# Optimization experiments

Measured on AMD Instinct MI355X. Metric: run time of the kernel, lower is better.

## Reference

```python
import jax, jax.numpy as jnp
import numpy as np

BS, NC, BH, BW, C = 1, 6, 100, 100, 256
HG, WG = 100, 40
HF, WF = 48, 80
HEADS, PTS, HD = 8, 8, 32
MAXOV = 2
NQ = HG * WG


def _nearest_sample(img, grid):
    # img: [B,H,W,Ch], grid: [B,Hg,Wg,2] in [-1,1]; nearest, align_corners=True, zeros padding
    B, H, W, _ = img.shape
    ix = jnp.round((grid[..., 0] + 1.0) * 0.5 * (W - 1))
    iy = jnp.round((grid[..., 1] + 1.0) * 0.5 * (H - 1))
    valid = (ix >= 0) & (ix <= W - 1) & (iy >= 0) & (iy <= H - 1)
    xc = jnp.clip(ix, 0, W - 1).astype(jnp.int32)
    yc = jnp.clip(iy, 0, H - 1).astype(jnp.int32)
    b = jnp.arange(B)[:, None, None]
    return img[b, yc, xc] * valid[..., None]


def _bilinear_sample(img, x, y):
    # img: [B,H,W,Ch]; x,y: [B,N] unnormalized (align_corners=False); zeros padding
    B, H, W, _ = img.shape
    x0 = jnp.floor(x)
    y0 = jnp.floor(y)
    wx1 = x - x0
    wy1 = y - y0
    b = jnp.arange(B)[:, None]

    def corner(xi, yi):
        valid = (xi >= 0) & (xi <= W - 1) & (yi >= 0) & (yi <= H - 1)
        xc = jnp.clip(xi, 0, W - 1).astype(jnp.int32)
        yc = jnp.clip(yi, 0, H - 1).astype(jnp.int32)
        return img[b, yc, xc] * valid[..., None]

    return (corner(x0, y0) * ((1 - wx1) * (1 - wy1))[..., None]
            + corner(x0 + 1, y0) * (wx1 * (1 - wy1))[..., None]
            + corner(x0, y0 + 1) * ((1 - wx1) * wy1)[..., None]
            + corner(x0 + 1, y0 + 1) * (wx1 * wy1)[..., None])


def _forward(query, value, queries_rebatch_grid, restore_bev_grid,
             reference_points_rebatch, bev_pillar_counts, query_pos,
             Wv, bv, Woff, boff, Watt, batt, Wout, bout, spatial_shapes):
    inp_residual = query
    q = query + query_pos                                       # [BS, BH*BW, C]
    # --- rebatch BEV queries per camera via nearest grid_sample ---
    qmap = jnp.broadcast_to(q.reshape(BS, 1, BH, BW, C),
                            (BS, NC, BH, BW, C)).reshape(BS * NC, BH, BW, C)
    q_reb = _nearest_sample(qmap, queries_rebatch_grid).reshape(BS * NC, NQ, C)
    ref = reference_points_rebatch.reshape(BS * NC, NQ, 2)      # flatten(-2): [BNC,NQ,2,1]->[BNC,NQ,2]
    # --- value projection ---
    v = value.transpose(2, 0, 1, 3).reshape(BS * NC, HF * WF, C)
    v = (v @ Wv + bv).reshape(BS * NC, HF, WF, HEADS, HD)
    # --- multi-scale deformable attention (single level) ---
    off = (q_reb @ Woff + boff).reshape(BS * NC, NQ, HEADS, PTS, 2)
    attw = jax.nn.softmax((q_reb @ Watt + batt).reshape(BS * NC, NQ, HEADS, PTS), axis=-1)
    normalizer = jnp.flip(spatial_shapes[0], 0).astype(jnp.float32)  # [WF, HF]
    loc = ref[:, :, None, None, :] + off / normalizer           # [BNC,NQ,HEADS,PTS,2] in [0,1]
    x = (loc[..., 0] * WF - 0.5).transpose(0, 2, 1, 3).reshape(BS * NC * HEADS, NQ * PTS)
    y = (loc[..., 1] * HF - 0.5).transpose(0, 2, 1, 3).reshape(BS * NC * HEADS, NQ * PTS)
    vh = v.transpose(0, 3, 1, 2, 4).reshape(BS * NC * HEADS, HF, WF, HD)
    samp = _bilinear_sample(vh, x, y).reshape(BS * NC, HEADS, NQ, PTS, HD)
    out = jnp.einsum('bhnpd,bnhp->bnhd', samp, attw).reshape(BS * NC, NQ, C)
    queries_out = out.transpose(0, 2, 1)                        # [BNC, C, NQ] (channels-first as module expects)
    # --- restore to BEV feature ---
    qo = queries_out.reshape(BS, NC, C, NQ).transpose(0, 2, 1, 3).reshape(BS, C, NC * HG, WG)
    bevq = _nearest_sample(qo.transpose(0, 2, 3, 1), restore_bev_grid)  # [BS, MAXOV*BH, BW, C]
    bevq = bevq.transpose(0, 3, 1, 2)                           # [BS, C, MAXOV*BH, BW]
    # reshape(BS, C*MAXOV, BH, BW) + all-ones grouped 1x1 conv == sum of the two overlap copies
    slots = bevq[:, :, :BH, :] + bevq[:, :, BH:, :]             # [BS, C, BH, BW]
    slots = slots.reshape(BS, C, BH * BW).transpose(0, 2, 1)    # [BS, BH*BW, C]
    slots = slots * bev_pillar_counts
    slots = slots @ Wout + bout
    return slots + inp_residual  # dropout identity in eval


def setup_inputs():
    key = jax.random.key(0)
    ks = jax.random.split(key, 14)
    s = 1.0 / np.sqrt(C)
    return {
        "query": jax.random.normal(ks[0], (BS, BH * BW, C), jnp.float32),
        "value": jax.random.normal(ks[1], (BS, HF * WF, NC, C), jnp.float32),
        "queries_rebatch_grid": jax.random.uniform(ks[2], (BS * NC, HG, WG, 2), jnp.float32, -1.0, 1.0),
        "restore_bev_grid": jax.random.uniform(ks[3], (BS, MAXOV * BH, BW, 2), jnp.float32, -1.0, 1.0),
        "reference_points_rebatch": jax.random.uniform(ks[4], (BS * NC, NQ, 2, 1), jnp.float32),
        "bev_pillar_counts": jax.random.uniform(ks[5], (BS, BH * BW, 1), jnp.float32),
        "query_pos": jax.random.normal(ks[6], (BS, BH * BW, C), jnp.float32),
        "Wv": jax.random.uniform(ks[7], (C, C), jnp.float32, -s, s),
        "bv": jnp.zeros((C,), jnp.float32),
        "Woff": jax.random.normal(ks[8], (C, HEADS * PTS * 2), jnp.float32) * 0.01,
        "boff": jax.random.uniform(ks[9], (HEADS * PTS * 2,), jnp.float32, -2.0, 2.0),
        "Watt": jax.random.normal(ks[10], (C, HEADS * PTS), jnp.float32) * 0.01,
        "batt": jnp.zeros((HEADS * PTS,), jnp.float32),
        "Wout": jax.random.uniform(ks[11], (C, C), jnp.float32, -s, s),
        "bout": jnp.zeros((C,), jnp.float32),
        "spatial_shapes": jnp.array([[HF, WF]], dtype=jnp.int32),
    }


def reference(query, value, queries_rebatch_grid, restore_bev_grid,
              reference_points_rebatch, bev_pillar_counts, query_pos,
              Wv, bv, Woff, boff, Watt, batt, Wout, bout, spatial_shapes):
    return _forward(query, value, queries_rebatch_grid, restore_bev_grid,
                    reference_points_rebatch, bev_pillar_counts, query_pos,
                    Wv, bv, Woff, boff, Watt, batt, Wout, bout, spatial_shapes)
```

## Files before the change

kernel.cpp:

```cpp
#include <hip/hip_runtime.h>
#include <hip/hip_bf16.h>
#include <math.h>

#define NCAMS 6
#define BH_ 100
#define BW_ 100
#define CDIM 256
#define NQ_ 4000
#define HF_ 48
#define WF_ 80
#define HEADS_ 8
#define PTS_ 8
#define HD_ 32
#define HWV (HF_*WF_)
#define M1_ (NCAMS*HWV)
#define M2_ (NCAMS*NQ_)
#define NOUT_ 10000

#define SA 264
#define SOFF 132
#define SATT 68

typedef __bf16 bf16_t;
typedef __bf16 bf16x8 __attribute__((ext_vector_type(8)));
typedef __bf16 bf16x4 __attribute__((ext_vector_type(4)));
typedef float  f32x4  __attribute__((ext_vector_type(4)));

static __device__ __forceinline__ f32x4 mfma16(bf16x8 a, bf16x8 b, f32x4 c) {
    return __builtin_amdgcn_mfma_f32_16x16x32_bf16(a, b, c, 0, 0, 0);
}

__global__ __launch_bounds__(256) void k0_prep(const float* __restrict__ Wv,
                                               const float* __restrict__ Woff,
                                               const float* __restrict__ Watt,
                                               const float* __restrict__ Wout,
                                               bf16_t* __restrict__ WvT,
                                               bf16_t* __restrict__ WcombT,
                                               bf16_t* __restrict__ WoutT) {
    int b = blockIdx.x, k = threadIdx.x;
    if (b < 256) {
        WvT[b * 256 + k] = (bf16_t)Wv[k * 256 + b];
    } else if (b < 448) {
        int n = b - 256;
        float v = (n < 128) ? Woff[k * 128 + n] : Watt[k * 64 + (n - 128)];
        WcombT[n * 256 + k] = (bf16_t)v;
    } else {
        int n = b - 448;
        WoutT[n * 256 + k] = (bf16_t)Wout[k * 256 + n];
    }
}

__global__ __launch_bounds__(256) void k1_vproj(const float* __restrict__ value,
                                                const bf16_t* __restrict__ WvT,
                                                const float* __restrict__ bv,
                                                bf16_t* __restrict__ vh) {
    __shared__ __align__(16) bf16_t At[32 * SA];
    const int m0 = blockIdx.x * 32;
    const int cam = m0 / HWV;
    const int hw0 = m0 - cam * HWV;
    for (int idx = threadIdx.x; idx < 32 * 64; idx += 256) {
        int r = idx >> 6, c4 = idx & 63;
        float4 v = ((const float4*)value)[((hw0 + r) * NCAMS + cam) * 64 + c4];
        bf16x4 pk; pk[0] = (bf16_t)v.x; pk[1] = (bf16_t)v.y; pk[2] = (bf16_t)v.z; pk[3] = (bf16_t)v.w;
        *(bf16x4*)(At + r * SA + c4 * 4) = pk;
    }
    __syncthreads();
    const int lane = threadIdx.x & 63, w = threadIdx.x >> 6;
    const int lr = lane & 15, lk = lane >> 4;
    f32x4 acc[2][4] = {};
    const bf16_t* a0 = At + lr * SA + lk * 8;
    const bf16_t* b0 = WvT + (w * 64 + lr) * 256 + lk * 8;
#pragma unroll
    for (int ks = 0; ks < 8; ++ks) {
        bf16x8 af[2], bf_[4];
#pragma unroll
        for (int mm = 0; mm < 2; ++mm) af[mm] = *(const bf16x8*)(a0 + mm * 16 * SA + ks * 32);
#pragma unroll
        for (int n = 0; n < 4; ++n) bf_[n] = *(const bf16x8*)(b0 + n * 16 * 256 + ks * 32);
#pragma unroll
        for (int mm = 0; mm < 2; ++mm)
#pragma unroll
            for (int n = 0; n < 4; ++n)
                acc[mm][n] = mfma16(af[mm], bf_[n], acc[mm][n]);
    }
    __syncthreads();
#pragma unroll
    for (int n = 0; n < 4; ++n) {
        int col = w * 64 + n * 16 + lr;
        float bias = bv[col];
#pragma unroll
        for (int mm = 0; mm < 2; ++mm)
#pragma unroll
            for (int j = 0; j < 4; ++j)
                At[(mm * 16 + lk * 4 + j) * SA + col] = (bf16_t)(acc[mm][n][j] + bias);
    }
    __syncthreads();
    for (int idx = threadIdx.x; idx < 32 * 32; idx += 256) {
        int r = idx >> 5, g = idx & 31;
        int head = g >> 2, part = g & 3;
        bf16x8 v = *(const bf16x8*)(At + r * SA + g * 8);
        *(bf16x8*)(vh + ((size_t)(cam * HEADS_ + head) * HWV + hw0 + r) * HD_ + part * 8) = v;
    }
}

__global__ __launch_bounds__(256) void k23_offatt_sample(
        const float* __restrict__ query,
        const float* __restrict__ qpos,
        const float* __restrict__ qgrid,
        const bf16_t* __restrict__ WcombT,
        const float* __restrict__ boff,
        const float* __restrict__ batt,
        const float* __restrict__ refp,
        const bf16_t* __restrict__ vh,
        bf16_t* __restrict__ out_attn) {
    __shared__ __align__(16) char u_lds[16 * SOFF * 4 + 16 * SATT * 4];
    bf16_t* At   = (bf16_t*)u_lds;
    float*  offs = (float*)u_lds;
    float*  atts = (float*)(u_lds + 16 * SOFF * 4);
    __shared__ int rowpos[16];
    __shared__ float rref[16][2];

    const int orig = blockIdx.x;
    const int xcd = orig & 7, idx8 = orig >> 3;
    const int lb = (xcd < 4 ? xcd * 188 : 4 * 188 + (xcd - 4) * 187) + idx8;
    const int m0 = lb * 16;
    const int cam = m0 / NQ_;

    if (threadIdx.x < 16) {
        int m = m0 + threadIdx.x;
        float gx = qgrid[m * 2 + 0], gy = qgrid[m * 2 + 1];
        float fx = rintf(__fmul_rn(__fmul_rn(__fadd_rn(gx, 1.0f), 0.5f), 99.0f));
        float fy = rintf(__fmul_rn(__fmul_rn(__fadd_rn(gy, 1.0f), 0.5f), 99.0f));
        bool valid = (fx >= 0.0f) && (fx <= 99.0f) && (fy >= 0.0f) && (fy <= 99.0f);
        rowpos[threadIdx.x] = valid ? ((int)fy * BW_ + (int)fx) : -1;
    } else if (threadIdx.x < 48) {
        int t = threadIdx.x - 16;
        rref[t >> 1][t & 1] = refp[(m0 + (t >> 1)) * 2 + (t & 1)];
    }
    __syncthreads();
    const float4* q4 = (const float4*)query;
    const float4* p4 = (const float4*)qpos;
    {
        int idx = threadIdx.x;
#pragma unroll
        for (int it = 0; it < 4; ++it, idx += 256) {
            int r = idx >> 6, c4 = idx & 63;
            int p = rowpos[r];
            bf16x4 pk;
            if (p >= 0) {
                float4 a = q4[p * 64 + c4];
                float4 b = p4[p * 64 + c4];
                pk[0] = (bf16_t)(a.x + b.x); pk[1] = (bf16_t)(a.y + b.y);
                pk[2] = (bf16_t)(a.z + b.z); pk[3] = (bf16_t)(a.w + b.w);
            } else {
                pk[0] = (bf16_t)0.0f; pk[1] = (bf16_t)0.0f; pk[2] = (bf16_t)0.0f; pk[3] = (bf16_t)0.0f;
            }
            *(bf16x4*)(At + r * SA + c4 * 4) = pk;
        }
    }
    __syncthreads();
    const int lane = threadIdx.x & 63, w = threadIdx.x >> 6;
    const int lr = lane & 15, lk = lane >> 4;
    const int wcol0 = w * 48;
    f32x4 acc[3] = {};
    {
        const bf16_t* a0 = At + lr * SA + lk * 8;
        const bf16_t* b0 = WcombT + (wcol0 + lr) * 256 + lk * 8;
#pragma unroll
        for (int ks = 0; ks < 8; ++ks) {
            bf16x8 af = *(const bf16x8*)(a0 + ks * 32);
            bf16x8 bf_[3];
#pragma unroll
            for (int n = 0; n < 3; ++n) bf_[n] = *(const bf16x8*)(b0 + n * 16 * 256 + ks * 32);
#pragma unroll
            for (int n = 0; n < 3; ++n)
                acc[n] = mfma16(af, bf_[n], acc[n]);
        }
    }
    __syncthreads();
#pragma unroll
    for (int n = 0; n < 3; ++n) {
        const int colbase = wcol0 + n * 16;
        const int col = colbase + lr;
        const int rloc = lk * 4;
        if (colbase < 128) {
            float bo = boff[col];
#pragma unroll
            for (int j = 0; j < 4; ++j)
                offs[(rloc + j) * SOFF + col] = acc[n][j] + bo;
        } else {
            float bt = batt[col - 128];
#pragma unroll
            for (int j = 0; j < 4; ++j) {
                float lg = acc[n][j] + bt;
                float mx = lg;
                mx = fmaxf(mx, __shfl_xor(mx, 1, 64));
                mx = fmaxf(mx, __shfl_xor(mx, 2, 64));
                mx = fmaxf(mx, __shfl_xor(mx, 4, 64));
                float e = expf(lg - mx);
                float s = e;
                s += __shfl_xor(s, 1, 64);
                s += __shfl_xor(s, 2, 64);
                s += __shfl_xor(s, 4, 64);
                atts[(rloc + j) * SATT + (col - 128)] = e / s;
            }
        }
    }
    __syncthreads();
    const int j = threadIdx.x & 3;
#pragma unroll
    for (int rep = 0; rep < 2; ++rep) {
        const int unit = rep * 64 + (threadIdx.x >> 2);
        const int r = unit >> 3, h = unit & 7;
        const int m = m0 + r;
        const float rx = rref[r][0];
        const float ry = rref[r][1];
        const bf16_t* base = vh + (size_t)(cam * HEADS_ + h) * HWV * HD_ + j * 8;
        const float4* off4 = (const float4*)(offs + r * SOFF + h * 16);
        const float4* att4 = (const float4*)(atts + r * SATT + h * 8);
        float4 o0 = off4[0], o1 = off4[1], o2 = off4[2], o3 = off4[3];
        float4 a0 = att4[0], a1 = att4[1];
        float offv[16] = {o0.x, o0.y, o0.z, o0.w, o1.x, o1.y, o1.z, o1.w,
                          o2.x, o2.y, o2.z, o2.w, o3.x, o3.y, o3.z, o3.w};
        float attv[8] = {a0.x, a0.y, a0.z, a0.w, a1.x, a1.y, a1.z, a1.w};
        float acc2[8] = {};
#pragma unroll
        for (int p = 0; p < PTS_; ++p) {
            float ax = fmaf(rx, (float)WF_, offv[p * 2 + 0] - 0.5f);
            float ay = fmaf(ry, (float)HF_, offv[p * 2 + 1] - 0.5f);
            float x0f = floorf(ax), y0f = floorf(ay);
            float wx = ax - x0f, wy = ay - y0f;
            float att = attv[p];
            bool vx0 = (x0f >= 0.0f) && (x0f <= (float)(WF_ - 1));
            bool vx1 = (x0f >= -1.0f) && (x0f <= (float)(WF_ - 2));
            bool vy0 = (y0f >= 0.0f) && (y0f <= (float)(HF_ - 1));
            bool vy1 = (y0f >= -1.0f) && (y0f <= (float)(HF_ - 2));
            float aw00 = (vx0 && vy0) ? att * (1.0f - wx) * (1.0f - wy) : 0.0f;
            float aw01 = (vx1 && vy0) ? att * wx * (1.0f - wy) : 0.0f;
            float aw10 = (vx0 && vy1) ? att * (1.0f - wx) * wy : 0.0f;
            float aw11 = (vx1 && vy1) ? att * wx * wy : 0.0f;
            int x0 = (int)fminf(fmaxf(x0f, 0.0f), (float)(WF_ - 1));
            int x1 = (int)fminf(fmaxf(x0f + 1.0f, 0.0f), (float)(WF_ - 1));
            int y0 = (int)fminf(fmaxf(y0f, 0.0f), (float)(HF_ - 1));
            int y1 = (int)fminf(fmaxf(y0f + 1.0f, 0.0f), (float)(HF_ - 1));
            bf16x8 c00 = *(const bf16x8*)(base + (y0 * WF_ + x0) * HD_);
            bf16x8 c01 = *(const bf16x8*)(base + (y0 * WF_ + x1) * HD_);
            bf16x8 c10 = *(const bf16x8*)(base + (y1 * WF_ + x0) * HD_);
            bf16x8 c11 = *(const bf16x8*)(base + (y1 * WF_ + x1) * HD_);
#pragma unroll
            for (int c = 0; c < 8; ++c) {
                acc2[c] = fmaf(aw00, (float)c00[c],
                          fmaf(aw01, (float)c01[c],
                          fmaf(aw10, (float)c10[c],
                          fmaf(aw11, (float)c11[c], acc2[c]))));
            }
        }
        bf16x8 ov;
#pragma unroll
        for (int c = 0; c < 8; ++c) ov[c] = (bf16_t)acc2[c];
        *(bf16x8*)(out_attn + (size_t)m * CDIM + h * HD_ + j * 8) = ov;
    }
}

__global__ __launch_bounds__(256) void k4_restore(const bf16_t* __restrict__ out_attn,
                                                  const float* __restrict__ rgrid,
                                                  const float* __restrict__ counts,
                                                  const bf16_t* __restrict__ WoutT,
                                                  const float* __restrict__ bout,
                                                  const float* __restrict__ query,
                                                  float* __restrict__ out) {
    __shared__ __align__(16) bf16_t At[32 * SA];
    __shared__ int pos2[32][2];
    __shared__ float cnt[32];
    const int m0 = blockIdx.x * 32;
    if (threadIdx.x < 64) {
        int r = threadIdx.x >> 1, k = threadIdx.x & 1;
        int i = m0 + r;
        if (i < NOUT_) {
            int bh = i / 100, bw = i - bh * 100;
            int R = bh + k * BH_;
            float gx = rgrid[(R * 100 + bw) * 2 + 0], gy = rgrid[(R * 100 + bw) * 2 + 1];
            float fx = rintf(__fmul_rn(__fmul_rn(__fadd_rn(gx, 1.0f), 0.5f), 39.0f));
            float fy = rintf(__fmul_rn(__fmul_rn(__fadd_rn(gy, 1.0f), 0.5f), 599.0f));
            bool valid = (fx >= 0.0f) && (fx <= 39.0f) && (fy >= 0.0f) && (fy <= 599.0f);
            int ix = (int)fx, iy = (int)fy;
            int camr = iy / 100, hg = iy - camr * 100;
            pos2[r][k] = valid ? (camr * NQ_ + hg * 40 + ix) : -1;
            if (k == 0) cnt[r] = counts[i];
        } else {
            pos2[r][k] = -1;
            if (k == 0) cnt[r] = 0.0f;
        }
    }
    __syncthreads();
    for (int idx = threadIdx.x; idx < 32 * 32; idx += 256) {
        int r = idx >> 5, g = idx & 31;
        int p0 = pos2[r][0], p1 = pos2[r][1];
        float s[8] = {};
        if (p0 >= 0) {
            bf16x8 a = *(const bf16x8*)(out_attn + (size_t)p0 * CDIM + g * 8);
#pragma unroll
            for (int c = 0; c < 8; ++c) s[c] += (float)a[c];
        }
        if (p1 >= 0) {
            bf16x8 a = *(const bf16x8*)(out_attn + (size_t)p1 * CDIM + g * 8);
#pragma unroll
            for (int c = 0; c < 8; ++c) s[c] += (float)a[c];
        }
        float cn = cnt[r];
        bf16x8 pk;
#pragma unroll
        for (int c = 0; c < 8; ++c) pk[c] = (bf16_t)(s[c] * cn);
        *(bf16x8*)(At + r * SA + g * 8) = pk;
    }
    __syncthreads();
    const int lane = threadIdx.x & 63, w = threadIdx.x >> 6;
    const int lr = lane & 15, lk = lane >> 4;
    f32x4 acc[2][4] = {};
    const bf16_t* a0 = At + lr * SA + lk * 8;
    const bf16_t* b0 = WoutT + (w * 64 + lr) * 256 + lk * 8;
#pragma unroll
    for (int ks = 0; ks < 8; ++ks) {
        bf16x8 af[2], bf_[4];
#pragma unroll
        for (int mm = 0; mm < 2; ++mm) af[mm] = *(const bf16x8*)(a0 + mm * 16 * SA + ks * 32);
#pragma unroll
        for (int n = 0; n < 4; ++n) bf_[n] = *(const bf16x8*)(b0 + n * 16 * 256 + ks * 32);
#pragma unroll
        for (int mm = 0; mm < 2; ++mm)
#pragma unroll
            for (int n = 0; n < 4; ++n)
                acc[mm][n] = mfma16(af[mm], bf_[n], acc[mm][n]);
    }
#pragma unroll
    for (int n = 0; n < 4; ++n) {
        int col = w * 64 + n * 16 + lr;
        float bo = bout[col];
#pragma unroll
        for (int mm = 0; mm < 2; ++mm)
#pragma unroll
            for (int j = 0; j < 4; ++j) {
                int row = m0 + mm * 16 + lk * 4 + j;
                if (row < NOUT_)
                    out[row * CDIM + col] = acc[mm][n][j] + bo + query[row * CDIM + col];
            }
    }
}

extern "C" void kernel_launch(void* const* d_in, const int* in_sizes, int n_in,
                              void* d_out, int out_size, void* d_ws, size_t ws_size,
                              hipStream_t stream) {
    (void)in_sizes; (void)n_in; (void)out_size; (void)ws_size;
    const float* query  = (const float*)d_in[0];
    const float* value  = (const float*)d_in[1];
    const float* qgrid  = (const float*)d_in[2];
    const float* rgrid  = (const float*)d_in[3];
    const float* refp   = (const float*)d_in[4];
    const float* counts = (const float*)d_in[5];
    const float* qpos   = (const float*)d_in[6];
    const float* Wv     = (const float*)d_in[7];
    const float* bv     = (const float*)d_in[8];
    const float* Woff   = (const float*)d_in[9];
    const float* boff   = (const float*)d_in[10];
    const float* Watt   = (const float*)d_in[11];
    const float* batt   = (const float*)d_in[12];
    const float* Wout   = (const float*)d_in[13];
    const float* bout   = (const float*)d_in[14];
    float* out = (float*)d_out;
    char* w8 = (char*)d_ws;

    bf16_t* vh       = (bf16_t*)(w8);
    bf16_t* out_attn = (bf16_t*)(w8 + 11796480);
    bf16_t* WvT      = (bf16_t*)(w8 + 24084480);
    bf16_t* WcombT   = (bf16_t*)(w8 + 24215552);
    bf16_t* WoutT    = (bf16_t*)(w8 + 24313856);

    hipLaunchKernelGGL(k0_prep,   dim3(704),      dim3(256), 0, stream, Wv, Woff, Watt, Wout,
                       WvT, WcombT, WoutT);
    hipLaunchKernelGGL(k1_vproj,  dim3(M1_ / 32), dim3(256), 0, stream, value, WvT, bv, vh);
    hipLaunchKernelGGL(k23_offatt_sample, dim3(M2_ / 16), dim3(256), 0, stream,
                       query, qpos, qgrid, WcombT, boff, batt, refp, vh, out_attn);
    hipLaunchKernelGGL(k4_restore, dim3(313),     dim3(256), 0, stream, out_attn, rgrid, counts,
                       WoutT, bout, query, out);
}
```

Baseline: 95.25 us.

## Precompute bf16 query+pos once and interleave two rows per sampling thread

The prep kernel now computes query+query_pos once per BEV cell and stores it as bf16, so the fused offset/attention kernel gathers 16-byte bf16 rows instead of two float4 streams per rebatched query. Because six cameras reuse the same BEV cells, this cuts redundant global reads and conversions. The sampling loop also processes two query rows per thread in one unrolled pass, issuing eight independent gathers at once for more memory-level parallelism. The cost is extra workspace, a larger prep launch, and higher register pressure in the sampling kernel.

```diff
diff --git a/kernel.cpp b/kernel.cpp
--- a/kernel.cpp
+++ b/kernel.cpp
@@ -34,9 +34,12 @@
                                                const float* __restrict__ Woff,
                                                const float* __restrict__ Watt,
                                                const float* __restrict__ Wout,
+                                               const float* __restrict__ query,
+                                               const float* __restrict__ qpos,
                                                bf16_t* __restrict__ WvT,
                                                bf16_t* __restrict__ WcombT,
-                                               bf16_t* __restrict__ WoutT) {
+                                               bf16_t* __restrict__ WoutT,
+                                               bf16_t* __restrict__ qsum) {
     int b = blockIdx.x, k = threadIdx.x;
     if (b < 256) {
         WvT[b * 256 + k] = (bf16_t)Wv[k * 256 + b];
@@ -44,9 +47,19 @@
         int n = b - 256;
         float v = (n < 128) ? Woff[k * 128 + n] : Watt[k * 64 + (n - 128)];
         WcombT[n * 256 + k] = (bf16_t)v;
-    } else {
+    } else if (b < 704) {
         int n = b - 448;
         WoutT[n * 256 + k] = (bf16_t)Wout[k * 256 + n];
+    } else {
+        int row0 = (b - 704) * 4;
+        int r = k >> 6, c4 = k & 63;
+        int i = (row0 + r) * 64 + c4;
+        float4 a = ((const float4*)query)[i];
+        float4 p = ((const float4*)qpos)[i];
+        bf16x4 pk;
+        pk[0] = (bf16_t)(a.x + p.x); pk[1] = (bf16_t)(a.y + p.y);
+        pk[2] = (bf16_t)(a.z + p.z); pk[3] = (bf16_t)(a.w + p.w);
+        *(bf16x4*)(qsum + (size_t)i * 4) = pk;
     }
 }
 
@@ -104,8 +117,7 @@
 }
 
 __global__ __launch_bounds__(256) void k23_offatt_sample(
-        const float* __restrict__ query,
-        const float* __restrict__ qpos,
+        const bf16_t* __restrict__ qsum,
         const float* __restrict__ qgrid,
         const bf16_t* __restrict__ WcombT,
         const float* __restrict__ boff,
@@ -138,24 +150,16 @@
         rref[t >> 1][t & 1] = refp[(m0 + (t >> 1)) * 2 + (t & 1)];
     }
     __syncthreads();
-    const float4* q4 = (const float4*)query;
-    const float4* p4 = (const float4*)qpos;
     {
         int idx = threadIdx.x;
 #pragma unroll
-        for (int it = 0; it < 4; ++it, idx += 256) {
-            int r = idx >> 6, c4 = idx & 63;
+        for (int it = 0; it < 2; ++it, idx += 256) {
+            int r = idx >> 5, g = idx & 31;
             int p = rowpos[r];
-            bf16x4 pk;
-            if (p >= 0) {
-                float4 a = q4[p * 64 + c4];
-                float4 b = p4[p * 64 + c4];
-                pk[0] = (bf16_t)(a.x + b.x); pk[1] = (bf16_t)(a.y + b.y);
-                pk[2] = (bf16_t)(a.z + b.z); pk[3] = (bf16_t)(a.w + b.w);
-            } else {
-                pk[0] = (bf16_t)0.0f; pk[1] = (bf16_t)0.0f; pk[2] = (bf16_t)0.0f; pk[3] = (bf16_t)0.0f;
-            }
-            *(bf16x4*)(At + r * SA + c4 * 4) = pk;
+            bf16x8 v;
+            if (p >= 0) v = *(const bf16x8*)(qsum + (size_t)p * 256 + g * 8);
+            else { bf16x8 z = {}; v = z; }
+            *(bf16x8*)(At + r * SA + g * 8) = v;
         }
     }
     __syncthreads();
@@ -208,58 +212,84 @@
     }
     __syncthreads();
     const int j = threadIdx.x & 3;
-#pragma unroll
-    for (int rep = 0; rep < 2; ++rep) {
-        const int unit = rep * 64 + (threadIdx.x >> 2);
-        const int r = unit >> 3, h = unit & 7;
-        const int m = m0 + r;
-        const float rx = rref[r][0];
-        const float ry = rref[r][1];
-        const bf16_t* base = vh + (size_t)(cam * HEADS_ + h) * HWV * HD_ + j * 8;
-        const float4* off4 = (const float4*)(offs + r * SOFF + h * 16);
-        const float4* att4 = (const float4*)(atts + r * SATT + h * 8);
-        float4 o0 = off4[0], o1 = off4[1], o2 = off4[2], o3 = off4[3];
-        float4 a0 = att4[0], a1 = att4[1];
-        float offv[16] = {o0.x, o0.y, o0.z, o0.w, o1.x, o1.y, o1.z, o1.w,
-                          o2.x, o2.y, o2.z, o2.w, o3.x, o3.y, o3.z, o3.w};
-        float attv[8] = {a0.x, a0.y, a0.z, a0.w, a1.x, a1.y, a1.z, a1.w};
-        float acc2[8] = {};
-#pragma unroll
-        for (int p = 0; p < PTS_; ++p) {
-            float ax = fmaf(rx, (float)WF_, offv[p * 2 + 0] - 0.5f);
-            float ay = fmaf(ry, (float)HF_, offv[p * 2 + 1] - 0.5f);
-            float x0f = floorf(ax), y0f = floorf(ay);
-            float wx = ax - x0f, wy = ay - y0f;
-            float att = attv[p];
-            bool vx0 = (x0f >= 0.0f) && (x0f <= (float)(WF_ - 1));
-            bool vx1 = (x0f >= -1.0f) && (x0f <= (float)(WF_ - 2));
-            bool vy0 = (y0f >= 0.0f) && (y0f <= (float)(HF_ - 1));
-            bool vy1 = (y0f >= -1.0f) && (y0f <= (float)(HF_ - 2));
-            float aw00 = (vx0 && vy0) ? att * (1.0f - wx) * (1.0f - wy) : 0.0f;
-            float aw01 = (vx1 && vy0) ? att * wx * (1.0f - wy) : 0.0f;
-            float aw10 = (vx0 && vy1) ? att * (1.0f - wx) * wy : 0.0f;
-            float aw11 = (vx1 && vy1) ? att * wx * wy : 0.0f;
-            int x0 = (int)fminf(fmaxf(x0f, 0.0f), (float)(WF_ - 1));
-            int x1 = (int)fminf(fmaxf(x0f + 1.0f, 0.0f), (float)(WF_ - 1));
-            int y0 = (int)fminf(fmaxf(y0f, 0.0f), (float)(HF_ - 1));
-            int y1 = (int)fminf(fmaxf(y0f + 1.0f, 0.0f), (float)(HF_ - 1));
-            bf16x8 c00 = *(const bf16x8*)(base + (y0 * WF_ + x0) * HD_);
-            bf16x8 c01 = *(const bf16x8*)(base + (y0 * WF_ + x1) * HD_);
-            bf16x8 c10 = *(const bf16x8*)(base + (y1 * WF_ + x0) * HD_);
-            bf16x8 c11 = *(const bf16x8*)(base + (y1 * WF_ + x1) * HD_);
-#pragma unroll
-            for (int c = 0; c < 8; ++c) {
-                acc2[c] = fmaf(aw00, (float)c00[c],
-                          fmaf(aw01, (float)c01[c],
-                          fmaf(aw10, (float)c10[c],
-                          fmaf(aw11, (float)c11[c], acc2[c]))));
-            }
-        }
-        bf16x8 ov;
-#pragma unroll
-        for (int c = 0; c < 8; ++c) ov[c] = (bf16_t)acc2[c];
-        *(bf16x8*)(out_attn + (size_t)m * CDIM + h * HD_ + j * 8) = ov;
-    }
+    const int u0 = threadIdx.x >> 2;
+    const int r0 = u0 >> 3, h = u0 & 7, r1 = r0 + 8;
+    const bf16_t* base = vh + (size_t)(cam * HEADS_ + h) * HWV * HD_ + j * 8;
+    const float rxA = rref[r0][0], ryA = rref[r0][1];
+    const float rxB = rref[r1][0], ryB = rref[r1][1];
+    const float4* offA4 = (const float4*)(offs + r0 * SOFF + h * 16);
+    const float4* offB4 = (const float4*)(offs + r1 * SOFF + h * 16);
+    float oA[16], oB[16];
+#pragma unroll
+    for (int q = 0; q < 4; ++q) {
+        float4 a = offA4[q], b = offB4[q];
+        oA[q * 4 + 0] = a.x; oA[q * 4 + 1] = a.y; oA[q * 4 + 2] = a.z; oA[q * 4 + 3] = a.w;
+        oB[q * 4 + 0] = b.x; oB[q * 4 + 1] = b.y; oB[q * 4 + 2] = b.z; oB[q * 4 + 3] = b.w;
+    }
+    const float* attA = atts + r0 * SATT + h * 8;
+    const float* attB = atts + r1 * SATT + h * 8;
+    float accA[8] = {}, accB[8] = {};
+#pragma unroll
+    for (int p = 0; p < PTS_; ++p) {
+        float axA = fmaf(rxA, (float)WF_, oA[p * 2 + 0] - 0.5f);
+        float ayA = fmaf(ryA, (float)HF_, oA[p * 2 + 1] - 0.5f);
+        float xA0f = floorf(axA), yA0f = floorf(ayA);
+        float wxA = axA - xA0f, wyA = ayA - yA0f;
+        float attA_p = attA[p];
+        bool vxA0 = (xA0f >= 0.0f) && (xA0f <= (float)(WF_ - 1));
+        bool vxA1 = (xA0f >= -1.0f) && (xA0f <= (float)(WF_ - 2));
+        bool vyA0 = (yA0f >= 0.0f) && (yA0f <= (float)(HF_ - 1));
+        bool vyA1 = (yA0f >= -1.0f) && (yA0f <= (float)(HF_ - 2));
+        float awA00 = (vxA0 && vyA0) ? attA_p * (1.0f - wxA) * (1.0f - wyA) : 0.0f;
+        float awA01 = (vxA1 && vyA0) ? attA_p * wxA * (1.0f - wyA) : 0.0f;
+        float awA10 = (vxA0 && vyA1) ? attA_p * (1.0f - wxA) * wyA : 0.0f;
+        float awA11 = (vxA1 && vyA1) ? attA_p * wxA * wyA : 0.0f;
+        int xA0 = (int)fminf(fmaxf(xA0f, 0.0f), (float)(WF_ - 1));
+        int xA1 = (int)fminf(fmaxf(xA0f + 1.0f, 0.0f), (float)(WF_ - 1));
+        int yA0 = (int)fminf(fmaxf(yA0f, 0.0f), (float)(HF_ - 1));
+        int yA1 = (int)fminf(fmaxf(yA0f + 1.0f, 0.0f), (float)(HF_ - 1));
+        float axB = fmaf(rxB, (float)WF_, oB[p * 2 + 0] - 0.5f);
+        float ayB = fmaf(ryB, (float)HF_, oB[p * 2 + 1] - 0.5f);
+        float xB0f = floorf(axB), yB0f = floorf(ayB);
+        float wxB = axB - xB0f, wyB = ayB - yB0f;
+        float attB_p = attB[p];
+        bool vxB0 = (xB0f >= 0.0f) && (xB0f <= (float)(WF_ - 1));
+        bool vxB1 = (xB0f >= -1.0f) && (xB0f <= (float)(WF_ - 2));
+        bool vyB0 = (yB0f >= 0.0f) && (yB0f <= (float)(HF_ - 1));
+        bool vyB1 = (yB0f >= -1.0f) && (yB0f <= (float)(HF_ - 2));
+        float awB00 = (vxB0 && vyB0) ? attB_p * (1.0f - wxB) * (1.0f - wyB) : 0.0f;
+        float awB01 = (vxB1 && vyB0) ? attB_p * wxB * (1.0f - wyB) : 0.0f;
+        float awB10 = (vxB0 && vyB1) ? attB_p * (1.0f - wxB) * wyB : 0.0f;
+        float awB11 = (vxB1 && vyB1) ? attB_p * wxB * wyB : 0.0f;
+        int xB0 = (int)fminf(fmaxf(xB0f, 0.0f), (float)(WF_ - 1));
+        int xB1 = (int)fminf(fmaxf(xB0f + 1.0f, 0.0f), (float)(WF_ - 1));
+        int yB0 = (int)fminf(fmaxf(yB0f, 0.0f), (float)(HF_ - 1));
+        int yB1 = (int)fminf(fmaxf(yB0f + 1.0f, 0.0f), (float)(HF_ - 1));
+        bf16x8 cA00 = *(const bf16x8*)(base + (yA0 * WF_ + xA0) * HD_);
+        bf16x8 cA01 = *(const bf16x8*)(base + (yA0 * WF_ + xA1) * HD_);
+        bf16x8 cA10 = *(const bf16x8*)(base + (yA1 * WF_ + xA0) * HD_);
+        bf16x8 cA11 = *(const bf16x8*)(base + (yA1 * WF_ + xA1) * HD_);
+        bf16x8 cB00 = *(const bf16x8*)(base + (yB0 * WF_ + xB0) * HD_);
+        bf16x8 cB01 = *(const bf16x8*)(base + (yB0 * WF_ + xB1) * HD_);
+        bf16x8 cB10 = *(const bf16x8*)(base + (yB1 * WF_ + xB0) * HD_);
+        bf16x8 cB11 = *(const bf16x8*)(base + (yB1 * WF_ + xB1) * HD_);
+#pragma unroll
+        for (int c = 0; c < 8; ++c) {
+            accA[c] = fmaf(awA00, (float)cA00[c],
+                      fmaf(awA01, (float)cA01[c],
+                      fmaf(awA10, (float)cA10[c],
+                      fmaf(awA11, (float)cA11[c], accA[c]))));
+            accB[c] = fmaf(awB00, (float)cB00[c],
+                      fmaf(awB01, (float)cB01[c],
+                      fmaf(awB10, (float)cB10[c],
+                      fmaf(awB11, (float)cB11[c], accB[c]))));
+        }
+    }
+    bf16x8 ovA, ovB;
+#pragma unroll
+    for (int c = 0; c < 8; ++c) { ovA[c] = (bf16_t)accA[c]; ovB[c] = (bf16_t)accB[c]; }
+    *(bf16x8*)(out_attn + (size_t)(m0 + r0) * CDIM + h * HD_ + j * 8) = ovA;
+    *(bf16x8*)(out_attn + (size_t)(m0 + r1) * CDIM + h * HD_ + j * 8) = ovB;
 }
 
 __global__ __launch_bounds__(256) void k4_restore(const bf16_t* __restrict__ out_attn,
@@ -374,12 +404,13 @@
     bf16_t* WvT      = (bf16_t*)(w8 + 24084480);
     bf16_t* WcombT   = (bf16_t*)(w8 + 24215552);
     bf16_t* WoutT    = (bf16_t*)(w8 + 24313856);
-
-    hipLaunchKernelGGL(k0_prep,   dim3(704),      dim3(256), 0, stream, Wv, Woff, Watt, Wout,
-                       WvT, WcombT, WoutT);
+    bf16_t* qsum     = (bf16_t*)(w8 + 24444928);
+
+    hipLaunchKernelGGL(k0_prep,   dim3(3204),     dim3(256), 0, stream, Wv, Woff, Watt, Wout,
+                       query, qpos, WvT, WcombT, WoutT, qsum);
     hipLaunchKernelGGL(k1_vproj,  dim3(M1_ / 32), dim3(256), 0, stream, value, WvT, bv, vh);
     hipLaunchKernelGGL(k23_offatt_sample, dim3(M2_ / 16), dim3(256), 0, stream,
-                       query, qpos, qgrid, WcombT, boff, batt, refp, vh, out_attn);
+                       qsum, qgrid, WcombT, boff, batt, refp, vh, out_attn);
     hipLaunchKernelGGL(k4_restore, dim3(313),     dim3(256), 0, stream, out_attn, rgrid, counts,
                        WoutT, bout, query, out);
 }
```

Result: no change. 94.45 us (-0.8%).

## Precompute bf16 query+pos sum and shrink per-block row tiles across kernels

Applied to the files above, without the earlier changes.

The prep kernel now also computes query+query_pos once into a bf16 buffer. The sampling kernel gathers from it with 16-byte bf16 loads instead of reading two fp32 arrays per rebatched row. Row tiles are halved in three kernels to double the block count: value projection goes from 32 to 16 rows, offset/attention/sampling from 16 to 8 (MFMA still runs 16 rows with half padded), restore from 32 to 16. The goal is more parallelism and less gather traffic, at the cost of wasted MFMA work on padding rows and reloading weights more often per row.

```diff
diff --git a/kernel.cpp b/kernel.cpp
--- a/kernel.cpp
+++ b/kernel.cpp
@@ -34,9 +34,12 @@
                                                const float* __restrict__ Woff,
                                                const float* __restrict__ Watt,
                                                const float* __restrict__ Wout,
+                                               const float* __restrict__ query,
+                                               const float* __restrict__ qpos,
                                                bf16_t* __restrict__ WvT,
                                                bf16_t* __restrict__ WcombT,
-                                               bf16_t* __restrict__ WoutT) {
+                                               bf16_t* __restrict__ WoutT,
+                                               bf16_t* __restrict__ qsum) {
     int b = blockIdx.x, k = threadIdx.x;
     if (b < 256) {
         WvT[b * 256 + k] = (bf16_t)Wv[k * 256 + b];
@@ -44,9 +47,19 @@
         int n = b - 256;
         float v = (n < 128) ? Woff[k * 128 + n] : Watt[k * 64 + (n - 128)];
         WcombT[n * 256 + k] = (bf16_t)v;
-    } else {
+    } else if (b < 704) {
         int n = b - 448;
         WoutT[n * 256 + k] = (bf16_t)Wout[k * 256 + n];
+    } else {
+        int row0 = (b - 704) * 4;
+        int r = k >> 6, c4 = k & 63;
+        int i = (row0 + r) * 64 + c4;
+        float4 a = ((const float4*)query)[i];
+        float4 p = ((const float4*)qpos)[i];
+        bf16x4 pk;
+        pk[0] = (bf16_t)(a.x + p.x); pk[1] = (bf16_t)(a.y + p.y);
+        pk[2] = (bf16_t)(a.z + p.z); pk[3] = (bf16_t)(a.w + p.w);
+        *(bf16x4*)(qsum + (size_t)i * 4) = pk;
     }
 }
 
@@ -54,34 +67,35 @@
                                                 const bf16_t* __restrict__ WvT,
                                                 const float* __restrict__ bv,
                                                 bf16_t* __restrict__ vh) {
-    __shared__ __align__(16) bf16_t At[32 * SA];
-    const int m0 = blockIdx.x * 32;
+    __shared__ __align__(16) bf16_t At[16 * SA];
+    const int m0 = blockIdx.x * 16;
     const int cam = m0 / HWV;
     const int hw0 = m0 - cam * HWV;
-    for (int idx = threadIdx.x; idx < 32 * 64; idx += 256) {
-        int r = idx >> 6, c4 = idx & 63;
-        float4 v = ((const float4*)value)[((hw0 + r) * NCAMS + cam) * 64 + c4];
-        bf16x4 pk; pk[0] = (bf16_t)v.x; pk[1] = (bf16_t)v.y; pk[2] = (bf16_t)v.z; pk[3] = (bf16_t)v.w;
-        *(bf16x4*)(At + r * SA + c4 * 4) = pk;
+    {
+        int idx = threadIdx.x;
+#pragma unroll
+        for (int it = 0; it < 4; ++it, idx += 256) {
+            int r = idx >> 6, c4 = idx & 63;
+            float4 v = ((const float4*)value)[((hw0 + r) * NCAMS + cam) * 64 + c4];
+            bf16x4 pk; pk[0] = (bf16_t)v.x; pk[1] = (bf16_t)v.y; pk[2] = (bf16_t)v.z; pk[3] = (bf16_t)v.w;
+            *(bf16x4*)(At + r * SA + c4 * 4) = pk;
+        }
     }
     __syncthreads();
     const int lane = threadIdx.x & 63, w = threadIdx.x >> 6;
     const int lr = lane & 15, lk = lane >> 4;
-    f32x4 acc[2][4] = {};
+    f32x4 acc[4] = {};
     const bf16_t* a0 = At + lr * SA + lk * 8;
     const bf16_t* b0 = WvT + (w * 64 + lr) * 256 + lk * 8;
 #pragma unroll
     for (int ks = 0; ks < 8; ++ks) {
-        bf16x8 af[2], bf_[4];
-#pragma unroll
-        for (int mm = 0; mm < 2; ++mm) af[mm] = *(const bf16x8*)(a0 + mm * 16 * SA + ks * 32);
+        bf16x8 af = *(const bf16x8*)(a0 + ks * 32);
+        bf16x8 bf_[4];
 #pragma unroll
         for (int n = 0; n < 4; ++n) bf_[n] = *(const bf16x8*)(b0 + n * 16 * 256 + ks * 32);
 #pragma unroll
-        for (int mm = 0; mm < 2; ++mm)
-#pragma unroll
-            for (int n = 0; n < 4; ++n)
-                acc[mm][n] = mfma16(af[mm], bf_[n], acc[mm][n]);
+        for (int n = 0; n < 4; ++n)
+            acc[n] = mfma16(af, bf_[n], acc[n]);
     }
     __syncthreads();
 #pragma unroll
@@ -89,23 +103,24 @@
         int col = w * 64 + n * 16 + lr;
         float bias = bv[col];
 #pragma unroll
-        for (int mm = 0; mm < 2; ++mm)
-#pragma unroll
-            for (int j = 0; j < 4; ++j)
-                At[(mm * 16 + lk * 4 + j) * SA + col] = (bf16_t)(acc[mm][n][j] + bias);
-    }
-    __syncthreads();
-    for (int idx = threadIdx.x; idx < 32 * 32; idx += 256) {
-        int r = idx >> 5, g = idx & 31;
-        int head = g >> 2, part = g & 3;
-        bf16x8 v = *(const bf16x8*)(At + r * SA + g * 8);
-        *(bf16x8*)(vh + ((size_t)(cam * HEADS_ + head) * HWV + hw0 + r) * HD_ + part * 8) = v;
+        for (int j = 0; j < 4; ++j)
+            At[(lk * 4 + j) * SA + col] = (bf16_t)(acc[n][j] + bias);
+    }
+    __syncthreads();
+    {
+        int idx = threadIdx.x;
+#pragma unroll
+        for (int it = 0; it < 2; ++it, idx += 256) {
+            int r = idx >> 5, g = idx & 31;
+            int head = g >> 2, part = g & 3;
+            bf16x8 v = *(const bf16x8*)(At + r * SA + g * 8);
+            *(bf16x8*)(vh + ((size_t)(cam * HEADS_ + head) * HWV + hw0 + r) * HD_ + part * 8) = v;
+        }
     }
 }
 
 __global__ __launch_bounds__(256) void k23_offatt_sample(
-        const float* __restrict__ query,
-        const float* __restrict__ qpos,
+        const bf16_t* __restrict__ qsum,
         const float* __restrict__ qgrid,
         const bf16_t* __restrict__ WcombT,
         const float* __restrict__ boff,
@@ -113,49 +128,45 @@
         const float* __restrict__ refp,
         const bf16_t* __restrict__ vh,
         bf16_t* __restrict__ out_attn) {
-    __shared__ __align__(16) char u_lds[16 * SOFF * 4 + 16 * SATT * 4];
+    __shared__ __align__(16) char u_lds[16 * SA * 2];
     bf16_t* At   = (bf16_t*)u_lds;
     float*  offs = (float*)u_lds;
-    float*  atts = (float*)(u_lds + 16 * SOFF * 4);
+    float*  atts = (float*)(u_lds + 8 * SOFF * 4);
     __shared__ int rowpos[16];
-    __shared__ float rref[16][2];
+    __shared__ float rref[8][2];
 
     const int orig = blockIdx.x;
-    const int xcd = orig & 7, idx8 = orig >> 3;
-    const int lb = (xcd < 4 ? xcd * 188 : 4 * 188 + (xcd - 4) * 187) + idx8;
-    const int m0 = lb * 16;
+    const int lb = (orig & 7) * 375 + (orig >> 3);
+    const int m0 = lb * 8;
     const int cam = m0 / NQ_;
 
     if (threadIdx.x < 16) {
-        int m = m0 + threadIdx.x;
-        float gx = qgrid[m * 2 + 0], gy = qgrid[m * 2 + 1];
-        float fx = rintf(__fmul_rn(__fmul_rn(__fadd_rn(gx, 1.0f), 0.5f), 99.0f));
-        float fy = rintf(__fmul_rn(__fmul_rn(__fadd_rn(gy, 1.0f), 0.5f), 99.0f));
-        bool valid = (fx >= 0.0f) && (fx <= 99.0f) && (fy >= 0.0f) && (fy <= 99.0f);
-        rowpos[threadIdx.x] = valid ? ((int)fy * BW_ + (int)fx) : -1;
-    } else if (threadIdx.x < 48) {
+        int r = threadIdx.x;
+        if (r < 8) {
+            int m = m0 + r;
+            float gx = qgrid[m * 2 + 0], gy = qgrid[m * 2 + 1];
+            float fx = rintf(__fmul_rn(__fmul_rn(__fadd_rn(gx, 1.0f), 0.5f), 99.0f));
+            float fy = rintf(__fmul_rn(__fmul_rn(__fadd_rn(gy, 1.0f), 0.5f), 99.0f));
+            bool valid = (fx >= 0.0f) && (fx <= 99.0f) && (fy >= 0.0f) && (fy <= 99.0f);
+            rowpos[r] = valid ? ((int)fy * BW_ + (int)fx) : -1;
+        } else {
+            rowpos[r] = -1;
+        }
+    } else if (threadIdx.x < 32) {
         int t = threadIdx.x - 16;
         rref[t >> 1][t & 1] = refp[(m0 + (t >> 1)) * 2 + (t & 1)];
     }
     __syncthreads();
-    const float4* q4 = (const float4*)query;
-    const float4* p4 = (const float4*)qpos;
     {
         int idx = threadIdx.x;
 #pragma unroll
-        for (int it = 0; it < 4; ++it, idx += 256) {
-            int r = idx >> 6, c4 = idx & 63;
+        for (int it = 0; it < 2; ++it, idx += 256) {
+            int r = idx >> 5, g = idx & 31;
             int p = rowpos[r];
-            bf16x4 pk;
-            if (p >= 0) {
-                float4 a = q4[p * 64 + c4];
-                float4 b = p4[p * 64 + c4];
-                pk[0] = (bf16_t)(a.x + b.x); pk[1] = (bf16_t)(a.y + b.y);
-                pk[2] = (bf16_t)(a.z + b.z); pk[3] = (bf16_t)(a.w + b.w);
-            } else {
-                pk[0] = (bf16_t)0.0f; pk[1] = (bf16_t)0.0f; pk[2] = (bf16_t)0.0f; pk[3] = (bf16_t)0.0f;
-            }
-            *(bf16x4*)(At + r * SA + c4 * 4) = pk;
+            bf16x8 v;
+            if (p >= 0) v = *(const bf16x8*)(qsum + (size_t)p * 256 + g * 8);
+            else { bf16x8 z = {}; v = z; }
+            *(bf16x8*)(At + r * SA + g * 8) = v;
         }
     }
     __syncthreads();
@@ -187,7 +198,8 @@
             float bo = boff[col];
 #pragma unroll
             for (int j = 0; j < 4; ++j)
-                offs[(rloc + j) * SOFF + col] = acc[n][j] + bo;
+                if (rloc + j < 8)
+                    offs[(rloc + j) * SOFF + col] = acc[n][j] + bo;
         } else {
             float bt = batt[col - 128];
 #pragma unroll
@@ -202,64 +214,62 @@
                 s += __shfl_xor(s, 1, 64);
                 s += __shfl_xor(s, 2, 64);
                 s += __shfl_xor(s, 4, 64);
-                atts[(rloc + j) * SATT + (col - 128)] = e / s;
+                if (rloc + j < 8)
+                    atts[(rloc + j) * SATT + (col - 128)] = e / s;
             }
         }
     }
     __syncthreads();
     const int j = threadIdx.x & 3;
-#pragma unroll
-    for (int rep = 0; rep < 2; ++rep) {
-        const int unit = rep * 64 + (threadIdx.x >> 2);
-        const int r = unit >> 3, h = unit & 7;
-        const int m = m0 + r;
-        const float rx = rref[r][0];
-        const float ry = rref[r][1];
-        const bf16_t* base = vh + (size_t)(cam * HEADS_ + h) * HWV * HD_ + j * 8;
-        const float4* off4 = (const float4*)(offs + r * SOFF + h * 16);
-        const float4* att4 = (const float4*)(atts + r * SATT + h * 8);
-        float4 o0 = off4[0], o1 = off4[1], o2 = off4[2], o3 = off4[3];
-        float4 a0 = att4[0], a1 = att4[1];
-        float offv[16] = {o0.x, o0.y, o0.z, o0.w, o1.x, o1.y, o1.z, o1.w,
-                          o2.x, o2.y, o2.z, o2.w, o3.x, o3.y, o3.z, o3.w};
-        float attv[8] = {a0.x, a0.y, a0.z, a0.w, a1.x, a1.y, a1.z, a1.w};
-        float acc2[8] = {};
-#pragma unroll
-        for (int p = 0; p < PTS_; ++p) {
-            float ax = fmaf(rx, (float)WF_, offv[p * 2 + 0] - 0.5f);
-            float ay = fmaf(ry, (float)HF_, offv[p * 2 + 1] - 0.5f);
-            float x0f = floorf(ax), y0f = floorf(ay);
-            float wx = ax - x0f, wy = ay - y0f;
-            float att = attv[p];
-            bool vx0 = (x0f >= 0.0f) && (x0f <= (float)(WF_ - 1));
-            bool vx1 = (x0f >= -1.0f) && (x0f <= (float)(WF_ - 2));
-            bool vy0 = (y0f >= 0.0f) && (y0f <= (float)(HF_ - 1));
-            bool vy1 = (y0f >= -1.0f) && (y0f <= (float)(HF_ - 2));
-            float aw00 = (vx0 && vy0) ? att * (1.0f - wx) * (1.0f - wy) : 0.0f;
-            float aw01 = (vx1 && vy0) ? att * wx * (1.0f - wy) : 0.0f;
-            float aw10 = (vx0 && vy1) ? att * (1.0f - wx) * wy : 0.0f;
-            float aw11 = (vx1 && vy1) ? att * wx * wy : 0.0f;
-            int x0 = (int)fminf(fmaxf(x0f, 0.0f), (float)(WF_ - 1));
-            int x1 = (int)fminf(fmaxf(x0f + 1.0f, 0.0f), (float)(WF_ - 1));
-            int y0 = (int)fminf(fmaxf(y0f, 0.0f), (float)(HF_ - 1));
-            int y1 = (int)fminf(fmaxf(y0f + 1.0f, 0.0f), (float)(HF_ - 1));
-            bf16x8 c00 = *(const bf16x8*)(base + (y0 * WF_ + x0) * HD_);
-            bf16x8 c01 = *(const bf16x8*)(base + (y0 * WF_ + x1) * HD_);
-            bf16x8 c10 = *(const bf16x8*)(base + (y1 * WF_ + x0) * HD_);
-            bf16x8 c11 = *(const bf16x8*)(base + (y1 * WF_ + x1) * HD_);
-#pragma unroll
-            for (int c = 0; c < 8; ++c) {
-                acc2[c] = fmaf(aw00, (float)c00[c],
-                          fmaf(aw01, (float)c01[c],
-                          fmaf(aw10, (float)c10[c],
-                          fmaf(aw11, (float)c11[c], acc2[c]))));
-            }
-        }
-        bf16x8 ov;
-#pragma unroll
-        for (int c = 0; c < 8; ++c) ov[c] = (bf16_t)acc2[c];
-        *(bf16x8*)(out_attn + (size_t)m * CDIM + h * HD_ + j * 8) = ov;
-    }
+    const int unit = threadIdx.x >> 2;
+    const int r0 = unit >> 3, h = unit & 7;
+    const int m = m0 + r0;
+    const bf16_t* base = vh + (size_t)(cam * HEADS_ + h) * HWV * HD_ + j * 8;
+    const float rx = rref[r0][0], ry = rref[r0][1];
+    const float4* off4 = (const float4*)(offs + r0 * SOFF + h * 16);
+    float offv[16];
+#pragma unroll
+    for (int q = 0; q < 4; ++q) {
+        float4 a = off4[q];
+        offv[q * 4 + 0] = a.x; offv[q * 4 + 1] = a.y; offv[q * 4 + 2] = a.z; offv[q * 4 + 3] = a.w;
+    }
+    const float* attp = atts + r0 * SATT + h * 8;
+    float acc2[8] = {};
+#pragma unroll
+    for (int p = 0; p < PTS_; ++p) {
+        float ax = fmaf(rx, (float)WF_, offv[p * 2 + 0] - 0.5f);
+        float ay = fmaf(ry, (float)HF_, offv[p * 2 + 1] - 0.5f);
+        float x0f = floorf(ax), y0f = floorf(ay);
+        float wx = ax - x0f, wy = ay - y0f;
+        float att = attp[p];
+        bool vx0 = (x0f >= 0.0f) && (x0f <= (float)(WF_ - 1));
+        bool vx1 = (x0f >= -1.0f) && (x0f <= (float)(WF_ - 2));
+        bool vy0 = (y0f >= 0.0f) && (y0f <= (float)(HF_ - 1));
+        bool vy1 = (y0f >= -1.0f) && (y0f <= (float)(HF_ - 2));
+        float aw00 = (vx0 && vy0) ? att * (1.0f - wx) * (1.0f - wy) : 0.0f;
+        float aw01 = (vx1 && vy0) ? att * wx * (1.0f - wy) : 0.0f;
+        float aw10 = (vx0 && vy1) ? att * (1.0f - wx) * wy : 0.0f;
+        float aw11 = (vx1 && vy1) ? att * wx * wy : 0.0f;
+        int x0 = (int)fminf(fmaxf(x0f, 0.0f), (float)(WF_ - 1));
+        int x1 = (int)fminf(fmaxf(x0f + 1.0f, 0.0f), (float)(WF_ - 1));
+        int y0 = (int)fminf(fmaxf(y0f, 0.0f), (float)(HF_ - 1));
+        int y1 = (int)fminf(fmaxf(y0f + 1.0f, 0.0f), (float)(HF_ - 1));
+        bf16x8 c00 = *(const bf16x8*)(base + (y0 * WF_ + x0) * HD_);
+        bf16x8 c01 = *(const bf16x8*)(base + (y0 * WF_ + x1) * HD_);
+        bf16x8 c10 = *(const bf16x8*)(base + (y1 * WF_ + x0) * HD_);
+        bf16x8 c11 = *(const bf16x8*)(base + (y1 * WF_ + x1) * HD_);
+#pragma unroll
+        for (int c = 0; c < 8; ++c) {
+            acc2[c] = fmaf(aw00, (float)c00[c],
+                      fmaf(aw01, (float)c01[c],
+                      fmaf(aw10, (float)c10[c],
+                      fmaf(aw11, (float)c11[c], acc2[c]))));
+        }
+    }
+    bf16x8 ov;
+#pragma unroll
+    for (int c = 0; c < 8; ++c) ov[c] = (bf16_t)acc2[c];
+    *(bf16x8*)(out_attn + (size_t)m * CDIM + h * HD_ + j * 8) = ov;
 }
 
 __global__ __launch_bounds__(256) void k4_restore(const bf16_t* __restrict__ out_attn,
@@ -269,81 +279,74 @@
                                                   const float* __restrict__ bout,
                                                   const float* __restrict__ query,
                                                   float* __restrict__ out) {
-    __shared__ __align__(16) bf16_t At[32 * SA];
-    __shared__ int pos2[32][2];
-    __shared__ float cnt[32];
-    const int m0 = blockIdx.x * 32;
-    if (threadIdx.x < 64) {
+    __shared__ __align__(16) bf16_t At[16 * SA];
+    __shared__ int pos2[16][2];
+    __shared__ float cnt[16];
+    const int m0 = blockIdx.x * 16;
+    if (threadIdx.x < 32) {
         int r = threadIdx.x >> 1, k = threadIdx.x & 1;
         int i = m0 + r;
-        if (i < NOUT_) {
-            int bh = i / 100, bw = i - bh * 100;
-            int R = bh + k * BH_;
-            float gx = rgrid[(R * 100 + bw) * 2 + 0], gy = rgrid[(R * 100 + bw) * 2 + 1];
-            float fx = rintf(__fmul_rn(__fmul_rn(__fadd_rn(gx, 1.0f), 0.5f), 39.0f));
-            float fy = rintf(__fmul_rn(__fmul_rn(__fadd_rn(gy, 1.0f), 0.5f), 599.0f));
-            bool valid = (fx >= 0.0f) && (fx <= 39.0f) && (fy >= 0.0f) && (fy <= 599.0f);
-            int ix = (int)fx, iy = (int)fy;
-            int camr = iy / 100, hg = iy - camr * 100;
-            pos2[r][k] = valid ? (camr * NQ_ + hg * 40 + ix) : -1;
-            if (k == 0) cnt[r] = counts[i];
-        } else {
-            pos2[r][k] = -1;
-            if (k == 0) cnt[r] = 0.0f;
-        }
-    }
-    __syncthreads();
-    for (int idx = threadIdx.x; idx < 32 * 32; idx += 256) {
-        int r = idx >> 5, g = idx & 31;
-        int p0 = pos2[r][0], p1 = pos2[r][1];
-        float s[8] = {};
-        if (p0 >= 0) {
-            bf16x8 a = *(const bf16x8*)(out_attn + (size_t)p0 * CDIM + g * 8);
-#pragma unroll
-            for (int c = 0; c < 8; ++c) s[c] += (float)a[c];
-        }
-        if (p1 >= 0) {
-            bf16x8 a = *(const bf16x8*)(out_attn + (size_t)p1 * CDIM + g * 8);
-#pragma unroll
-            for (int c = 0; c < 8; ++c) s[c] += (float)a[c];
-        }
-        float cn = cnt[r];
-        bf16x8 pk;
-#pragma unroll
-        for (int c = 0; c < 8; ++c) pk[c] = (bf16_t)(s[c] * cn);
-        *(bf16x8*)(At + r * SA + g * 8) = pk;
+        int bh = i / 100, bw = i - bh * 100;
+        int R = bh + k * BH_;
+        float gx = rgrid[(R * 100 + bw) * 2 + 0], gy = rgrid[(R * 100 + bw) * 2 + 1];
+        float fx = rintf(__fmul_rn(__fmul_rn(__fadd_rn(gx, 1.0f), 0.5f), 39.0f));
+        float fy = rintf(__fmul_rn(__fmul_rn(__fadd_rn(gy, 1.0f), 0.5f), 599.0f));
+        bool valid = (fx >= 0.0f) && (fx <= 39.0f) && (fy >= 0.0f) && (fy <= 599.0f);
+        int ix = (int)fx, iy = (int)fy;
+        int camr = iy / 100, hg = iy - camr * 100;
+        pos2[r][k] = valid ? (camr * NQ_ + hg * 40 + ix) : -1;
+        if (k == 0) cnt[r] = counts[i];
+    }
+    __syncthreads();
+    {
+        int idx = threadIdx.x;
+#pragma unroll
+        for (int it = 0; it < 2; ++it, idx += 256) {
+            int r = idx >> 5, g = idx & 31;
+            int p0 = pos2[r][0], p1 = pos2[r][1];
+            float s[8] = {};
+            if (p0 >= 0) {
+                bf16x8 a = *(const bf16x8*)(out_attn + (size_t)p0 * CDIM + g * 8);
+#pragma unroll
+                for (int c = 0; c < 8; ++c) s[c] += (float)a[c];
+            }
+            if (p1 >= 0) {
+                bf16x8 a = *(const bf16x8*)(out_attn + (size_t)p1 * CDIM + g * 8);
+#pragma unroll
+                for (int c = 0; c < 8; ++c) s[c] += (float)a[c];
+            }
+            float cn = cnt[r];
+            bf16x8 pk;
+#pragma unroll
+            for (int c = 0; c < 8; ++c) pk[c] = (bf16_t)(s[c] * cn);
+            *(bf16x8*)(At + r * SA + g * 8) = pk;
+        }
     }
     __syncthreads();
     const int lane = threadIdx.x & 63, w = threadIdx.x >> 6;
     const int lr = lane & 15, lk = lane >> 4;
-    f32x4 acc[2][4] = {};
+    f32x4 acc[4] = {};
     const bf16_t* a0 = At + lr * SA + lk * 8;
     const bf16_t* b0 = WoutT + (w * 64 + lr) * 256 + lk * 8;
 #pragma unroll
     for (int ks = 0; ks < 8; ++ks) {
-        bf16x8 af[2], bf_[4];
-#pragma unroll
-        for (int mm = 0; mm < 2; ++mm) af[mm] = *(const bf16x8*)(a0 + mm * 16 * SA + ks * 32);
+        bf16x8 af = *(const bf16x8*)(a0 + ks * 32);
+        bf16x8 bf_[4];
 #pragma unroll
         for (int n = 0; n < 4; ++n) bf_[n] = *(const bf16x8*)(b0 + n * 16 * 256 + ks * 32);
 #pragma unroll
-        for (int mm = 0; mm < 2; ++mm)
-#pragma unroll
-            for (int n = 0; n < 4; ++n)
-                acc[mm][n] = mfma16(af[mm], bf_[n], acc[mm][n]);
+        for (int n = 0; n < 4; ++n)
+            acc[n] = mfma16(af, bf_[n], acc[n]);
     }
 #pragma unroll
     for (int n = 0; n < 4; ++n) {
         int col = w * 64 + n * 16 + lr;
         float bo = bout[col];
 #pragma unroll
-        for (int mm = 0; mm < 2; ++mm)
-#pragma unroll
-            for (int j = 0; j < 4; ++j) {
-                int row = m0 + mm * 16 + lk * 4 + j;
-                if (row < NOUT_)
-                    out[row * CDIM + col] = acc[mm][n][j] + bo + query[row * CDIM + col];
-            }
+        for (int j = 0; j < 4; ++j) {
+            int row = m0 + lk * 4 + j;
+            out[row * CDIM + col] = acc[n][j] + bo + query[row * CDIM + col];
+        }
     }
 }
 
@@ -374,12 +377,13 @@
     bf16_t* WvT      = (bf16_t*)(w8 + 24084480);
     bf16_t* WcombT   = (bf16_t*)(w8 + 24215552);
     bf16_t* WoutT    = (bf16_t*)(w8 + 24313856);
-
-    hipLaunchKernelGGL(k0_prep,   dim3(704),      dim3(256), 0, stream, Wv, Woff, Watt, Wout,
-                       WvT, WcombT, WoutT);
-    hipLaunchKernelGGL(k1_vproj,  dim3(M1_ / 32), dim3(256), 0, stream, value, WvT, bv, vh);
-    hipLaunchKernelGGL(k23_offatt_sample, dim3(M2_ / 16), dim3(256), 0, stream,
-                       query, qpos, qgrid, WcombT, boff, batt, refp, vh, out_attn);
-    hipLaunchKernelGGL(k4_restore, dim3(313),     dim3(256), 0, stream, out_attn, rgrid, counts,
+    bf16_t* qsum     = (bf16_t*)(w8 + 24444928);
+
+    hipLaunchKernelGGL(k0_prep,   dim3(3204),     dim3(256), 0, stream, Wv, Woff, Watt, Wout,
+                       query, qpos, WvT, WcombT, WoutT, qsum);
+    hipLaunchKernelGGL(k1_vproj,  dim3(M1_ / 16), dim3(256), 0, stream, value, WvT, bv, vh);
+    hipLaunchKernelGGL(k23_offatt_sample, dim3(3000), dim3(256), 0, stream,
+                       qsum, qgrid, WcombT, boff, batt, refp, vh, out_attn);
+    hipLaunchKernelGGL(k4_restore, dim3(625),     dim3(256), 0, stream, out_attn, rgrid, counts,
                        WoutT, bout, query, out);
 }
```

Result: slower. 112.9 us (+18.5%).
